# Optimization experiments

Measured on AMD Instinct MI355X. Metric: run time of the kernel, lower is better.

## Reference

```python
import jax, jax.numpy as jnp
import numpy as np


def setup_inputs() -> dict:
    key = jax.random.key(0)
    ks = jax.random.split(key, 6)
    B, H, W, Cin, Cout, wdim = 8, 64, 64, 512, 512, 512
    return {
        "x": jax.random.normal(ks[0], (B, H, W, Cin), jnp.float32),
        "w": jax.random.normal(ks[1], (B, wdim), jnp.float32),
        "noise": jax.random.normal(ks[2], (B, H, W, 1), jnp.float32),
        "style_weight": jax.random.normal(ks[3], (wdim, Cin), jnp.float32),
        "style_bias": jnp.ones((Cin,), jnp.float32),
        "conv_weight": jax.random.normal(ks[4], (3, 3, Cin, Cout), jnp.float32),
        "scale_noise": 0.1 * jax.random.normal(ks[5], (1, 1, 1, Cout), jnp.float32),
        "bias": jax.random.normal(jax.random.fold_in(key, 7), (Cout,), jnp.float32),
    }


def reference(x, w, noise, style_weight, style_bias, conv_weight, scale_noise, bias):
    wdim = style_weight.shape[0]
    kh, kw, cin, cout = conv_weight.shape
    # Equalized-LR fully connected to_style (gain=1, lr_mult=1, bias init ones,
    # activation=True -> leaky_relu(0.2) with sqrt(2) gain, StyleGAN2 convention).
    s = w @ (style_weight * (1.0 / np.sqrt(wdim))) + style_bias  # [B, Cin]
    s = jax.nn.leaky_relu(s, 0.2) * np.sqrt(2.0).astype(np.float32)
    # Modulated conv (demodulated). Equalized-LR weight scale 1/sqrt(fan_in).
    wk = conv_weight * (1.0 / np.sqrt(kh * kw * cin))  # [3,3,Cin,Cout]
    # demod[b,o] = rsqrt(sum_{h,w,i} (wk[h,w,i,o]*s[b,i])^2 + eps)
    d = jax.lax.rsqrt(jnp.einsum('hwio,bi->bo', wk * wk, s * s) + 1e-8)  # [B,Cout]
    xm = x * s[:, None, None, :]  # modulate inputs instead of per-sample weights
    y = jax.lax.conv_general_dilated(
        xm, wk, window_strides=(1, 1), padding='SAME',
        dimension_numbers=('NHWC', 'HWIO', 'NHWC'))
    y = y * d[:, None, None, :]
    # noise scale-add + bias + leaky-relu (the fused tail in StyleGAN2 kernels)
    y = y + scale_noise * noise + bias
    return jax.nn.leaky_relu(y, 0.2)
```

## Files before the change

kernel.cpp:

```cpp
#include <hip/hip_runtime.h>
#include <hip/hip_bf16.h>
#include <stdint.h>


typedef __attribute__((ext_vector_type(8))) __bf16 bf16x8;
typedef __attribute__((ext_vector_type(16))) float f32x16;

__device__ __forceinline__ float bf2f(ushort u) {
    union { uint32_t i; float f; } v; v.i = (uint32_t)u << 16; return v.f;
}
__device__ __forceinline__ ushort f2bf(float f) {
    union { float f; uint32_t i; } v; v.f = f;
    uint32_t r = v.i + 0x7fffu + ((v.i >> 16) & 1u);
    return (ushort)(r >> 16);
}
__device__ __forceinline__ int sniff_f32(const void* sb) {
    return ((const uint32_t*)sb)[0] == 0x3F800000u;
}
__device__ __forceinline__ float lda(const void* p, int idx, int isf) {
    return isf ? ((const float*)p)[idx] : bf2f(((const ushort*)p)[idx]);
}

union U16x8 { uint4 v; ushort u[8]; };

#define INV_SQRT_WDIM 0.04419417382415922f
#define SQRT2         1.4142135623730951f
#define WSCALE        0.014731391274719739f

__global__ void k_style_part(const void* __restrict__ w, const void* __restrict__ sw,
                             const void* __restrict__ sb, float* __restrict__ part) {
    int isf = sniff_f32(sb);
    int b = blockIdx.x >> 3, ds = blockIdx.x & 7;
    int i = threadIdx.x;
    __shared__ float wrow[64];
    if (i < 64) wrow[i] = lda(w, b * 512 + ds * 64 + i, isf);
    __syncthreads();
    float acc = 0.f;
    if (isf) {
        const float* p = (const float*)sw + (size_t)ds * 64 * 512;
#pragma unroll 8
        for (int d = 0; d < 64; ++d) acc += wrow[d] * p[d * 512 + i];
    } else {
        const ushort* p = (const ushort*)sw + (size_t)ds * 64 * 512;
#pragma unroll 8
        for (int d = 0; d < 64; ++d) acc += wrow[d] * bf2f(p[d * 512 + i]);
    }
    part[(b * 8 + ds) * 512 + i] = acc;
}

__global__ void k_style_fin(const float* __restrict__ part, const void* __restrict__ sb,
                            float* __restrict__ s_out) {
    int isf = sniff_f32(sb);
    int b = blockIdx.x, i = threadIdx.x;
    float a = 0.f;
#pragma unroll
    for (int ds = 0; ds < 8; ++ds) a += part[(b * 8 + ds) * 512 + i];
    float s = a * INV_SQRT_WDIM + lda(sb, i, isf);
    s = (s > 0.f ? s : 0.2f * s) * SQRT2;
    s_out[b * 512 + i] = s;
}

__global__ void k_pad(const void* __restrict__ x, const float* __restrict__ s,
                      const void* __restrict__ sb, ushort* __restrict__ xmp) {
    int isf = sniff_f32(sb);
    int pr = blockIdx.x;
    int b = pr / 66, yp = pr % 66;
    int tid = threadIdx.x;
    ushort* rowp = xmp + ((size_t)b * 66 + yp) * 66 * 512;
    uint4 z = {0u, 0u, 0u, 0u};
    if (yp == 0 || yp == 65) {
        uint4* p = (uint4*)rowp;
        for (int l = tid; l < 66 * 512 * 2 / 16; l += 256) p[l] = z;
        return;
    }
    __shared__ float sv[512];
    for (int c = tid; c < 512; c += 256) sv[c] = s[b * 512 + c];
    if (tid < 64)       ((uint4*)rowp)[tid] = z;
    else if (tid < 128) ((uint4*)(rowp + 65 * 512))[tid - 64] = z;
    __syncthreads();
    int y = yp - 1;
    ushort* xout = rowp + 512;
    if (isf) {
        const float* xin = (const float*)x + ((size_t)b * 64 + y) * 64 * 512;
        for (int l = tid; l < 8192; l += 256) {
            int xi = l >> 7, cc = (l & 127) * 4;
            float4 in = *(const float4*)(xin + (size_t)xi * 512 + cc);
            ushort4 ov;
            ov.x = f2bf(in.x * sv[cc + 0]);
            ov.y = f2bf(in.y * sv[cc + 1]);
            ov.z = f2bf(in.z * sv[cc + 2]);
            ov.w = f2bf(in.w * sv[cc + 3]);
            *(ushort4*)(xout + (size_t)xi * 512 + cc) = ov;
        }
    } else {
        const ushort* xin = (const ushort*)x + ((size_t)b * 64 + y) * 64 * 512;
        for (int l = tid; l < 4096; l += 256) {
            int xi = l >> 6, cc = (l & 63) * 8;
            U16x8 in, ov;
            in.v = *(const uint4*)(xin + (size_t)xi * 512 + cc);
#pragma unroll
            for (int j = 0; j < 8; ++j) ov.u[j] = f2bf(bf2f(in.u[j]) * sv[cc + j]);
            *(uint4*)(xout + (size_t)xi * 512 + cc) = ov.v;
        }
    }
}

__global__ void k_wt(const void* __restrict__ cw, const void* __restrict__ sb,
                     ushort* __restrict__ wkt2) {
    int isf = sniff_f32(sb);
    int bid = blockIdx.x;
    int t = bid / 64, ib = (bid % 64) / 8, ob = bid % 8;
    __shared__ ushort tile[64][65];
    int tid = threadIdx.x;
    int oq = tid & 15, ir = tid >> 4;
#pragma unroll
    for (int p = 0; p < 4; ++p) {
        int i = p * 16 + ir;
        size_t off = ((size_t)(t * 512 + ib * 64 + i)) * 512 + ob * 64 + oq * 4;
        float v0, v1, v2, v3;
        if (isf) {
            float4 v = *(const float4*)((const float*)cw + off);
            v0 = v.x; v1 = v.y; v2 = v.z; v3 = v.w;
        } else {
            ushort4 v = *(const ushort4*)((const ushort*)cw + off);
            v0 = bf2f(v.x); v1 = bf2f(v.y); v2 = bf2f(v.z); v3 = bf2f(v.w);
        }
        tile[i][oq * 4 + 0] = f2bf(v0 * WSCALE);
        tile[i][oq * 4 + 1] = f2bf(v1 * WSCALE);
        tile[i][oq * 4 + 2] = f2bf(v2 * WSCALE);
        tile[i][oq * 4 + 3] = f2bf(v3 * WSCALE);
    }
    __syncthreads();
    int kql = tid >> 6, ol = tid & 63;
    int kq = ib * 4 + kql;
    U16x8 lo, hi;
#pragma unroll
    for (int j = 0; j < 8; ++j) {
        lo.u[j] = tile[kql * 16 + j][ol];
        hi.u[j] = tile[kql * 16 + 8 + j][ol];
    }
    uint4* dst = (uint4*)(wkt2 + ((size_t)((t * 32 + kq) * 512) + ob * 64 + ol) * 16);
    dst[0] = lo.v;
    dst[1] = hi.v;
}

__global__ void k_dmod(const ushort* __restrict__ wkt2, const float* __restrict__ s,
                       float* __restrict__ part) {
    int t = blockIdx.x / 8, ob = blockIdx.x % 8;
    int tid = threadIdx.x;
    __shared__ float s2[4096];
    __shared__ float red[2048];
#pragma unroll
    for (int j = 0; j < 16; ++j) {
        int idx = j * 256 + tid;
        float v = s[idx];
        s2[idx] = v * v;
    }
    __syncthreads();
    int q = tid >> 6, ol = tid & 63;
    int o = ob * 64 + ol;
    float acc[8] = {0, 0, 0, 0, 0, 0, 0, 0};
    for (int kk = 0; kk < 8; ++kk) {
        int kq = q * 8 + kk;
        const uint4* p = (const uint4*)(wkt2 + ((size_t)((t * 32 + kq) * 512) + o) * 16);
        U16x8 w0, w1;
        w0.v = p[0];
        w1.v = p[1];
        int ibase = kq * 16;
#pragma unroll
        for (int e = 0; e < 8; ++e) {
            float wf = bf2f(w0.u[e]);
            float w2 = wf * wf;
#pragma unroll
            for (int b = 0; b < 8; ++b) acc[b] += w2 * s2[b * 512 + ibase + e];
        }
#pragma unroll
        for (int e = 0; e < 8; ++e) {
            float wf = bf2f(w1.u[e]);
            float w2 = wf * wf;
#pragma unroll
            for (int b = 0; b < 8; ++b) acc[b] += w2 * s2[b * 512 + ibase + 8 + e];
        }
    }
#pragma unroll
    for (int b = 0; b < 8; ++b) red[(ol * 8 + b) * 4 + q] = acc[b];
    __syncthreads();
#pragma unroll
    for (int p = 0; p < 2; ++p) {
        int qq = tid * 2 + p;
        int ol2 = qq >> 3, b2 = qq & 7;
        float sum = red[qq * 4 + 0] + red[qq * 4 + 1] + red[qq * 4 + 2] + red[qq * 4 + 3];
        part[(b2 * 9 + t) * 512 + ob * 64 + ol2] = sum;
    }
}

__global__ void k_dfin(const float* __restrict__ part, float* __restrict__ d) {
    int gid = blockIdx.x * 256 + threadIdx.x;
    int b = gid >> 9, o = gid & 511;
    float acc = 1e-8f;
#pragma unroll
    for (int t = 0; t < 9; ++t) acc += part[(b * 9 + t) * 512 + o];
    d[b * 512 + o] = rsqrtf(acc);
}

#define GLL(gp, lp) __builtin_amdgcn_global_load_lds( \
    (const __attribute__((address_space(1))) void*)(gp), \
    (__attribute__((address_space(3))) void*)(lp), 16, 0, 0)

__launch_bounds__(256, 2)
__global__ void k_conv(const ushort* __restrict__ xmp, const ushort* __restrict__ wkt2,
                       const float* __restrict__ dmod, const void* __restrict__ noise,
                       const void* __restrict__ snoise, const void* __restrict__ bias_,
                       const void* __restrict__ sb, void* __restrict__ out) {
    __shared__ ushort Ah[2][4 * 66 * 64];
    int isf = sniff_f32(sb);
    int id = blockIdx.x;
    int ct = id & 3;
    int rt = (id >> 2) & 31;
    int b  = id >> 7;
    int y0 = rt * 2, o0 = ct * 128;
    int tid = threadIdx.x;
    int lane = tid & 63, wv = tid >> 6;
    int wm = (wv >> 1) * 64, wn = (wv & 1) * 64;
    int lm = lane & 31, kh = lane >> 5;
    const ushort* xb = xmp + (size_t)b * 66 * 66 * 512;
    const char* bp = (const char*)wkt2;
    size_t boff = ((size_t)(o0 + wn + lm)) * 32 + (size_t)(kh * 16);

    f32x16 acc[2][2] = {};
    bf16x8 bA[2][4], bB[2][4];

    auto stageA = [&](int c0a, char* dstA) {
#pragma unroll
        for (int it = 0; it < 8; ++it) {
            int L = it * 256 + tid;
            int cidx = L >> 3, slot = L & 7;
            int hrow = cidx / 66, col = cidx - hrow * 66;
            int kc = slot ^ (col & 7);
            GLL(xb + ((size_t)(y0 + hrow) * 66 + col) * 512 + c0a + kc * 8,
                dstA + L * 16);
        }
        if (wv == 0) {
            int L = 2048 + tid;
            int cidx = L >> 3, slot = L & 7;
            int hrow = cidx / 66, col = cidx - hrow * 66;
            int kc = slot ^ (col & 7);
            GLL(xb + ((size_t)(y0 + hrow) * 66 + col) * 512 + c0a + kc * 8,
                dstA + L * 16);
        }
    };

    auto loadB = [&](int tt, int cc, bf16x8 (&dst)[2][4]) {
#pragma unroll
        for (int ks = 0; ks < 4; ++ks) {
            int kq = cc * 4 + ks;
            const char* pk = bp + (size_t)(tt * 32 + kq) * 16384 + boff;
            dst[0][ks] = *(const bf16x8*)(pk);
            dst[1][ks] = *(const bf16x8*)(pk + 1024);
        }
    };

    auto tap = [&](int t, const bf16x8 (&cur)[2][4], bf16x8 (&nxt)[2][4],
                   int pre_t, int pre_c, const char* AhC) {
        if (pre_t >= 0) loadB(pre_t, pre_c, nxt);
        int dy = t / 3 - 1, dx = t % 3 - 1;
        int hrow = (wv >> 1) + dy + 1;
#pragma unroll
        for (int ks = 0; ks < 4; ++ks) {
            int ck = ks * 2 + kh;
            bf16x8 afr[2];
#pragma unroll
            for (int am = 0; am < 2; ++am) {
                int col = am * 32 + lm + dx + 1;
                afr[am] = *(const bf16x8*)(AhC +
                    (((hrow * 66 + col) << 3) + (ck ^ (col & 7))) * 16);
            }
#pragma unroll
            for (int am = 0; am < 2; ++am)
#pragma unroll
                for (int bn = 0; bn < 2; ++bn)
                    acc[am][bn] = __builtin_amdgcn_mfma_f32_32x32x16_bf16(
                        afr[am], cur[bn][ks], acc[am][bn], 0, 0, 0);
        }
    };

    stageA(0, (char*)Ah[0]);
    loadB(0, 0, bA);
    __syncthreads();
    for (int c = 0; c < 8; ++c) {
        if (c < 7) stageA((c + 1) * 64, (char*)Ah[(c + 1) & 1]);
        const char* AhC = (const char*)Ah[c & 1];
        tap(0, bA, bB, 1, c, AhC);
        tap(1, bB, bA, 2, c, AhC);
        tap(2, bA, bB, 3, c, AhC);
        tap(3, bB, bA, 4, c, AhC);
        tap(4, bA, bB, 5, c, AhC);
        tap(5, bB, bA, 6, c, AhC);
        tap(6, bA, bB, 7, c, AhC);
        tap(7, bB, bA, 8, c, AhC);
        tap(8, bA, bB, (c < 7) ? 0 : -1, c + 1, AhC);
#pragma unroll
        for (int ks = 0; ks < 4; ++ks) {
            bA[0][ks] = bB[0][ks];
            bA[1][ks] = bB[1][ks];
        }
        __syncthreads();
    }

    float dv[2], snv[2], bv[2];
#pragma unroll
    for (int bn = 0; bn < 2; ++bn) {
        int o = o0 + wn + bn * 32 + lm;
        dv[bn] = dmod[b * 512 + o];
        snv[bn] = lda(snoise, o, isf);
        bv[bn] = lda(bias_, o, isf);
    }
#pragma unroll
    for (int am = 0; am < 2; ++am) {
#pragma unroll
        for (int reg = 0; reg < 16; ++reg) {
            int p = wm + am * 32 + 4 * kh + (reg & 3) + 8 * (reg >> 2);
            int yy = y0 + (p >> 6), xx = p & 63;
            float nz = lda(noise, (b * 64 + yy) * 64 + xx, isf);
            size_t obase = ((size_t)(b * 64 + yy) * 64 + xx) * 512;
            if (isf) {
                float* of = (float*)out;
#pragma unroll
                for (int bn = 0; bn < 2; ++bn) {
                    float v = acc[am][bn][reg] * dv[bn] + snv[bn] * nz + bv[bn];
                    v = v > 0.f ? v : 0.2f * v;
                    of[obase + o0 + wn + bn * 32 + lm] = v;
                }
            } else {
                ushort* ob = (ushort*)out;
#pragma unroll
                for (int bn = 0; bn < 2; ++bn) {
                    float v = acc[am][bn][reg] * dv[bn] + snv[bn] * nz + bv[bn];
                    v = v > 0.f ? v : 0.2f * v;
                    ob[obase + o0 + wn + bn * 32 + lm] = f2bf(v);
                }
            }
        }
    }
}

extern "C" void kernel_launch(void* const* d_in, const int* in_sizes, int n_in,
                              void* d_out, int out_size, void* d_ws, size_t ws_size,
                              hipStream_t stream) {
    const void* x     = d_in[0];
    const void* w     = d_in[1];
    const void* noise = d_in[2];
    const void* sw    = d_in[3];
    const void* sb    = d_in[4];
    const void* cw    = d_in[5];
    const void* sn    = d_in[6];
    const void* bias  = d_in[7];

    char* ws = (char*)d_ws;
    ushort* xmp   = (ushort*)(ws);
    ushort* wkt2  = (ushort*)(ws + 35684352);
    float*  s     = (float*)(ws + 40402944);
    float*  dmod  = (float*)(ws + 40419328);
    float*  part  = (float*)(ws + 40435712);
    float*  spart = (float*)(ws + 40583168);
    (void)in_sizes; (void)n_in; (void)out_size; (void)ws_size;

    hipLaunchKernelGGL(k_style_part, dim3(64),     dim3(512), 0, stream, w, sw, sb, spart);
    hipLaunchKernelGGL(k_style_fin,  dim3(8),      dim3(512), 0, stream, spart, sb, s);
    hipLaunchKernelGGL(k_wt,         dim3(576),    dim3(256), 0, stream, cw, sb, wkt2);
    hipLaunchKernelGGL(k_dmod,       dim3(72),     dim3(256), 0, stream, wkt2, s, part);
    hipLaunchKernelGGL(k_dfin,       dim3(16),     dim3(256), 0, stream, part, dmod);
    hipLaunchKernelGGL(k_pad,        dim3(8 * 66), dim3(256), 0, stream, x, s, sb, xmp);
    hipLaunchKernelGGL(k_conv,       dim3(1024),   dim3(256), 0, stream,
                       xmp, wkt2, dmod, noise, sn, bias, sb, d_out);
}
```

Before: 341.3 us.

## Restage conv weights through LDS with larger row tiles and triple-buffered pipeline

The conv kernel now covers four output rows per block instead of two, so each block issues twice as many MFMAs per loaded weight fragment. Weights move through a triple-buffered LDS ring filled by global_load_lds, with explicit vmcnt waits and barriers taking the place of direct register prefetch. The weight layout moves to 8-element K groups, the input tile uses 32-channel chunks without the XOR swizzle, and k_dmod now reads the raw conv weights. The grid shrinks to 512 blocks, and the larger accumulators and LDS footprint may lower occupancy, while the hand-tuned wait counts are fragile.

```diff
diff --git a/kernel.cpp b/kernel.cpp
--- a/kernel.cpp
+++ b/kernel.cpp
@@ -109,43 +109,30 @@
                      ushort* __restrict__ wkt2) {
     int isf = sniff_f32(sb);
     int bid = blockIdx.x;
-    int t = bid / 64, ib = (bid % 64) / 8, ob = bid % 8;
-    __shared__ ushort tile[64][65];
+    int t = bid / 64, ckg = bid % 64;
+    __shared__ ushort sm[8][512];
     int tid = threadIdx.x;
-    int oq = tid & 15, ir = tid >> 4;
-#pragma unroll
-    for (int p = 0; p < 4; ++p) {
-        int i = p * 16 + ir;
-        size_t off = ((size_t)(t * 512 + ib * 64 + i)) * 512 + ob * 64 + oq * 4;
-        float v0, v1, v2, v3;
-        if (isf) {
-            float4 v = *(const float4*)((const float*)cw + off);
-            v0 = v.x; v1 = v.y; v2 = v.z; v3 = v.w;
-        } else {
-            ushort4 v = *(const ushort4*)((const ushort*)cw + off);
-            v0 = bf2f(v.x); v1 = bf2f(v.y); v2 = bf2f(v.z); v3 = bf2f(v.w);
-        }
-        tile[i][oq * 4 + 0] = f2bf(v0 * WSCALE);
-        tile[i][oq * 4 + 1] = f2bf(v1 * WSCALE);
-        tile[i][oq * 4 + 2] = f2bf(v2 * WSCALE);
-        tile[i][oq * 4 + 3] = f2bf(v3 * WSCALE);
-    }
-    __syncthreads();
-    int kql = tid >> 6, ol = tid & 63;
-    int kq = ib * 4 + kql;
-    U16x8 lo, hi;
-#pragma unroll
-    for (int j = 0; j < 8; ++j) {
-        lo.u[j] = tile[kql * 16 + j][ol];
-        hi.u[j] = tile[kql * 16 + 8 + j][ol];
-    }
-    uint4* dst = (uint4*)(wkt2 + ((size_t)((t * 32 + kq) * 512) + ob * 64 + ol) * 16);
-    dst[0] = lo.v;
-    dst[1] = hi.v;
-}
-
-__global__ void k_dmod(const ushort* __restrict__ wkt2, const float* __restrict__ s,
-                       float* __restrict__ part) {
+#pragma unroll
+    for (int r = 0; r < 16; ++r) {
+        int l = r * 256 + tid;
+        int j = l >> 9, o = l & 511;
+        float v = lda(cw, (size_t)(t * 512 + ckg * 8 + j) * 512 + o, isf);
+        sm[j][o] = f2bf(v * WSCALE);
+    }
+    __syncthreads();
+#pragma unroll
+    for (int r = 0; r < 2; ++r) {
+        int o = r * 256 + tid;
+        U16x8 pk;
+#pragma unroll
+        for (int j = 0; j < 8; ++j) pk.u[j] = sm[j][o];
+        *(uint4*)(wkt2 + ((size_t)(t * 64 + ckg) * 512 + o) * 8) = pk.v;
+    }
+}
+
+__global__ void k_dmod(const void* __restrict__ cw, const void* __restrict__ sb,
+                       const float* __restrict__ s, float* __restrict__ part) {
+    int isf = sniff_f32(sb);
     int t = blockIdx.x / 8, ob = blockIdx.x % 8;
     int tid = threadIdx.x;
     __shared__ float s2[4096];
@@ -160,27 +147,12 @@
     int q = tid >> 6, ol = tid & 63;
     int o = ob * 64 + ol;
     float acc[8] = {0, 0, 0, 0, 0, 0, 0, 0};
-    for (int kk = 0; kk < 8; ++kk) {
-        int kq = q * 8 + kk;
-        const uint4* p = (const uint4*)(wkt2 + ((size_t)((t * 32 + kq) * 512) + o) * 16);
-        U16x8 w0, w1;
-        w0.v = p[0];
-        w1.v = p[1];
-        int ibase = kq * 16;
-#pragma unroll
-        for (int e = 0; e < 8; ++e) {
-            float wf = bf2f(w0.u[e]);
-            float w2 = wf * wf;
-#pragma unroll
-            for (int b = 0; b < 8; ++b) acc[b] += w2 * s2[b * 512 + ibase + e];
-        }
-#pragma unroll
-        for (int e = 0; e < 8; ++e) {
-            float wf = bf2f(w1.u[e]);
-            float w2 = wf * wf;
-#pragma unroll
-            for (int b = 0; b < 8; ++b) acc[b] += w2 * s2[b * 512 + ibase + 8 + e];
-        }
+    for (int ii = 0; ii < 128; ++ii) {
+        int i = q * 128 + ii;
+        float wf = lda(cw, (size_t)(t * 512 + i) * 512 + o, isf) * WSCALE;
+        float w2 = wf * wf;
+#pragma unroll
+        for (int b = 0; b < 8; ++b) acc[b] += w2 * s2[b * 512 + i];
     }
 #pragma unroll
     for (int b = 0; b < 8; ++b) red[(ol * 8 + b) * 4 + q] = acc[b];
@@ -206,121 +178,130 @@
 #define GLL(gp, lp) __builtin_amdgcn_global_load_lds( \
     (const __attribute__((address_space(1))) void*)(gp), \
     (__attribute__((address_space(3))) void*)(lp), 16, 0, 0)
+#define VW(n) asm volatile("s_waitcnt vmcnt(" #n ")" ::: "memory")
 
 __launch_bounds__(256, 2)
 __global__ void k_conv(const ushort* __restrict__ xmp, const ushort* __restrict__ wkt2,
                        const float* __restrict__ dmod, const void* __restrict__ noise,
                        const void* __restrict__ snoise, const void* __restrict__ bias_,
                        const void* __restrict__ sb, void* __restrict__ out) {
-    __shared__ ushort Ah[2][4 * 66 * 64];
+    __shared__ ushort Ah[2][1584 * 8];
+    __shared__ ushort Bb[3][512 * 8];
     int isf = sniff_f32(sb);
     int id = blockIdx.x;
     int ct = id & 3;
-    int rt = (id >> 2) & 31;
-    int b  = id >> 7;
-    int y0 = rt * 2, o0 = ct * 128;
+    int rt = (id >> 2) & 15;
+    int b  = id >> 6;
+    int y0 = rt * 4, o0 = ct * 128;
     int tid = threadIdx.x;
     int lane = tid & 63, wv = tid >> 6;
-    int wm = (wv >> 1) * 64, wn = (wv & 1) * 64;
+    int wr = wv >> 1, wc = wv & 1;
     int lm = lane & 31, kh = lane >> 5;
     const ushort* xb = xmp + (size_t)b * 66 * 66 * 512;
-    const char* bp = (const char*)wkt2;
-    size_t boff = ((size_t)(o0 + wn + lm)) * 32 + (size_t)(kh * 16);
-
-    f32x16 acc[2][2] = {};
-    bf16x8 bA[2][4], bB[2][4];
-
-    auto stageA = [&](int c0a, char* dstA) {
-#pragma unroll
-        for (int it = 0; it < 8; ++it) {
-            int L = it * 256 + tid;
-            int cidx = L >> 3, slot = L & 7;
-            int hrow = cidx / 66, col = cidx - hrow * 66;
-            int kc = slot ^ (col & 7);
-            GLL(xb + ((size_t)(y0 + hrow) * 66 + col) * 512 + c0a + kc * 8,
-                dstA + L * 16);
+    const ushort* wp = wkt2;
+
+    uint aoff[7];
+#pragma unroll
+    for (int it = 0; it < 7; ++it) {
+        int chunk = (it < 6) ? (it * 256 + tid) : (1536 + wv * 12 + lane);
+        int ck = chunk / 396;
+        int rem = chunk - ck * 396;
+        int hr = rem / 66, cl = rem - hr * 66;
+        aoff[it] = (uint)(((y0 + hr) * 66 + cl) * 512 + ck * 8);
+    }
+    uint boff[2];
+#pragma unroll
+    for (int it = 0; it < 2; ++it) {
+        int L = it * 256 + tid;
+        boff[it] = (uint)(((L >> 7) * 512 + o0 + (L & 127)) * 8);
+    }
+
+    auto stageA = [&](int c0a, int abuf) {
+        char* dstA = (char*)Ah[abuf];
+#pragma unroll
+        for (int it = 0; it < 6; ++it)
+            GLL(xb + aoff[it] + c0a, dstA + (it * 256 + tid) * 16);
+        if (lane < 12)
+            GLL(xb + aoff[6] + c0a, dstA + (1536 + wv * 12 + lane) * 16);
+    };
+    auto stageB = [&](int pb, int slot) {
+        char* dstB = (char*)Bb[slot];
+#pragma unroll
+        for (int it = 0; it < 2; ++it)
+            GLL(wp + (size_t)pb * 4096 + boff[it], dstB + (it * 256 + tid) * 16);
+    };
+
+    f32x16 acc[4][2] = {};
+
+    stageA(0, 0);
+    stageB(0 * 64 + 0, 0);
+    stageB(1 * 64 + 0, 1);
+    VW(2);
+    __builtin_amdgcn_s_barrier();
+    __builtin_amdgcn_sched_barrier(0);
+
+    for (int c = 0; c < 16; ++c) {
+        int c0 = c * 32;
+#pragma unroll
+        for (int t = 0; t < 9; ++t) {
+            if (!(c == 15 && t >= 7)) {
+                int tt2 = (t <= 6) ? (t + 2) : (t - 7);
+                int cc2 = (t <= 6) ? c : (c + 1);
+                stageB(tt2 * 64 + cc2 * 4, (t + 2) % 3);
+            }
+            if (t == 0 && c < 15) stageA(c0 + 32, (c + 1) & 1);
+
+            const char* AhC = (const char*)Ah[c & 1];
+            const char* BbC = (const char*)Bb[t % 3];
+            int dy = t / 3 - 1, dx = t % 3 - 1;
+            __builtin_amdgcn_s_setprio(1);
+#pragma unroll
+            for (int ks = 0; ks < 2; ++ks) {
+                bf16x8 afr[4], bfr[2];
+#pragma unroll
+                for (int am = 0; am < 4; ++am)
+                    afr[am] = *(const bf16x8*)(AhC + (ks * 2 + kh) * 6336
+                        + (wr * 2 + (am >> 1) + dy + 1) * 1056
+                        + ((am & 1) * 32 + lm + dx + 1) * 16);
+#pragma unroll
+                for (int bn = 0; bn < 2; ++bn)
+                    bfr[bn] = *(const bf16x8*)(BbC + (ks * 2 + kh) * 2048
+                        + (wc * 64 + bn * 32 + lm) * 16);
+#pragma unroll
+                for (int am = 0; am < 4; ++am)
+#pragma unroll
+                    for (int bn = 0; bn < 2; ++bn)
+                        acc[am][bn] = __builtin_amdgcn_mfma_f32_32x32x16_bf16(
+                            afr[am], bfr[bn], acc[am][bn], 0, 0, 0);
+            }
+            __builtin_amdgcn_s_setprio(0);
+
+            if (t <= 1)      { if (c < 15) { VW(9); } else { VW(2); } }
+            else if (t <= 6) { VW(2); }
+            else if (t == 7) { if (c < 15) { VW(2); } else { VW(0); } }
+            else             { if (c < 15) { VW(2); } }
+            if (!(c == 15 && t == 8)) {
+                __builtin_amdgcn_s_barrier();
+                __builtin_amdgcn_sched_barrier(0);
+            }
         }
-        if (wv == 0) {
-            int L = 2048 + tid;
-            int cidx = L >> 3, slot = L & 7;
-            int hrow = cidx / 66, col = cidx - hrow * 66;
-            int kc = slot ^ (col & 7);
-            GLL(xb + ((size_t)(y0 + hrow) * 66 + col) * 512 + c0a + kc * 8,
-                dstA + L * 16);
-        }
-    };
-
-    auto loadB = [&](int tt, int cc, bf16x8 (&dst)[2][4]) {
-#pragma unroll
-        for (int ks = 0; ks < 4; ++ks) {
-            int kq = cc * 4 + ks;
-            const char* pk = bp + (size_t)(tt * 32 + kq) * 16384 + boff;
-            dst[0][ks] = *(const bf16x8*)(pk);
-            dst[1][ks] = *(const bf16x8*)(pk + 1024);
-        }
-    };
-
-    auto tap = [&](int t, const bf16x8 (&cur)[2][4], bf16x8 (&nxt)[2][4],
-                   int pre_t, int pre_c, const char* AhC) {
-        if (pre_t >= 0) loadB(pre_t, pre_c, nxt);
-        int dy = t / 3 - 1, dx = t % 3 - 1;
-        int hrow = (wv >> 1) + dy + 1;
-#pragma unroll
-        for (int ks = 0; ks < 4; ++ks) {
-            int ck = ks * 2 + kh;
-            bf16x8 afr[2];
-#pragma unroll
-            for (int am = 0; am < 2; ++am) {
-                int col = am * 32 + lm + dx + 1;
-                afr[am] = *(const bf16x8*)(AhC +
-                    (((hrow * 66 + col) << 3) + (ck ^ (col & 7))) * 16);
-            }
-#pragma unroll
-            for (int am = 0; am < 2; ++am)
-#pragma unroll
-                for (int bn = 0; bn < 2; ++bn)
-                    acc[am][bn] = __builtin_amdgcn_mfma_f32_32x32x16_bf16(
-                        afr[am], cur[bn][ks], acc[am][bn], 0, 0, 0);
-        }
-    };
-
-    stageA(0, (char*)Ah[0]);
-    loadB(0, 0, bA);
-    __syncthreads();
-    for (int c = 0; c < 8; ++c) {
-        if (c < 7) stageA((c + 1) * 64, (char*)Ah[(c + 1) & 1]);
-        const char* AhC = (const char*)Ah[c & 1];
-        tap(0, bA, bB, 1, c, AhC);
-        tap(1, bB, bA, 2, c, AhC);
-        tap(2, bA, bB, 3, c, AhC);
-        tap(3, bB, bA, 4, c, AhC);
-        tap(4, bA, bB, 5, c, AhC);
-        tap(5, bB, bA, 6, c, AhC);
-        tap(6, bA, bB, 7, c, AhC);
-        tap(7, bB, bA, 8, c, AhC);
-        tap(8, bA, bB, (c < 7) ? 0 : -1, c + 1, AhC);
-#pragma unroll
-        for (int ks = 0; ks < 4; ++ks) {
-            bA[0][ks] = bB[0][ks];
-            bA[1][ks] = bB[1][ks];
-        }
-        __syncthreads();
     }
 
     float dv[2], snv[2], bv[2];
 #pragma unroll
     for (int bn = 0; bn < 2; ++bn) {
-        int o = o0 + wn + bn * 32 + lm;
+        int o = o0 + wc * 64 + bn * 32 + lm;
         dv[bn] = dmod[b * 512 + o];
         snv[bn] = lda(snoise, o, isf);
         bv[bn] = lda(bias_, o, isf);
     }
 #pragma unroll
-    for (int am = 0; am < 2; ++am) {
+    for (int am = 0; am < 4; ++am) {
 #pragma unroll
         for (int reg = 0; reg < 16; ++reg) {
-            int p = wm + am * 32 + 4 * kh + (reg & 3) + 8 * (reg >> 2);
-            int yy = y0 + (p >> 6), xx = p & 63;
+            int crow = 4 * kh + (reg & 3) + 8 * (reg >> 2);
+            int yy = y0 + wr * 2 + (am >> 1);
+            int xx = (am & 1) * 32 + crow;
             float nz = lda(noise, (b * 64 + yy) * 64 + xx, isf);
             size_t obase = ((size_t)(b * 64 + yy) * 64 + xx) * 512;
             if (isf) {
@@ -329,7 +310,7 @@
                 for (int bn = 0; bn < 2; ++bn) {
                     float v = acc[am][bn][reg] * dv[bn] + snv[bn] * nz + bv[bn];
                     v = v > 0.f ? v : 0.2f * v;
-                    of[obase + o0 + wn + bn * 32 + lm] = v;
+                    of[obase + o0 + wc * 64 + bn * 32 + lm] = v;
                 }
             } else {
                 ushort* ob = (ushort*)out;
@@ -337,7 +318,7 @@
                 for (int bn = 0; bn < 2; ++bn) {
                     float v = acc[am][bn][reg] * dv[bn] + snv[bn] * nz + bv[bn];
                     v = v > 0.f ? v : 0.2f * v;
-                    ob[obase + o0 + wn + bn * 32 + lm] = f2bf(v);
+                    ob[obase + o0 + wc * 64 + bn * 32 + lm] = f2bf(v);
                 }
             }
         }
@@ -368,9 +349,9 @@
     hipLaunchKernelGGL(k_style_part, dim3(64),     dim3(512), 0, stream, w, sw, sb, spart);
     hipLaunchKernelGGL(k_style_fin,  dim3(8),      dim3(512), 0, stream, spart, sb, s);
     hipLaunchKernelGGL(k_wt,         dim3(576),    dim3(256), 0, stream, cw, sb, wkt2);
-    hipLaunchKernelGGL(k_dmod,       dim3(72),     dim3(256), 0, stream, wkt2, s, part);
+    hipLaunchKernelGGL(k_dmod,       dim3(72),     dim3(256), 0, stream, cw, sb, s, part);
     hipLaunchKernelGGL(k_dfin,       dim3(16),     dim3(256), 0, stream, part, dmod);
     hipLaunchKernelGGL(k_pad,        dim3(8 * 66), dim3(256), 0, stream, x, s, sb, xmp);
-    hipLaunchKernelGGL(k_conv,       dim3(1024),   dim3(256), 0, stream,
+    hipLaunchKernelGGL(k_conv,       dim3(512),    dim3(256), 0, stream,
                        xmp, wkt2, dmod, noise, sn, bias, sb, d_out);
 }
```

New measurement: 337.7 us. Within noise of the previous version (-1.1%).
